# Performance work log

Measured on AMD Instinct MI355X. Metric: run time of the kernel, lower is better.

The kernel has to match this reference:

```python
import jax, jax.numpy as jnp
import numpy as np

VOCAB, DIM, B, S = 32000, 1024, 64, 512

def setup_inputs() -> dict:
    key = jax.random.key(0)
    ks = jax.random.split(key, 16)
    std = 1.0 / np.sqrt(DIM)
    return {
        "x": jax.random.randint(ks[0], (B,), 0, VOCAB),
        "h": jax.random.normal(ks[1], (B, DIM), jnp.float32),
        "c": jax.random.normal(ks[2], (B, DIM), jnp.float32),
        "enc_y": jax.random.normal(ks[3], (B, S, DIM), jnp.float32),
        "F_emb": jax.random.normal(ks[4], (VOCAB, DIM), jnp.float32),
        "W1_w": jax.random.uniform(ks[5], (DIM, DIM), jnp.float32, -std, std),
        "W1_b": jnp.zeros((DIM,), jnp.float32),
        "W2_w": jax.random.uniform(ks[6], (DIM, DIM), jnp.float32, -std, std),
        "W2_b": jnp.zeros((DIM,), jnp.float32),
        "V_w": jax.random.uniform(ks[7], (1, DIM), jnp.float32, -std, std),
        "V_b": jnp.zeros((1,), jnp.float32),
        "W_ih": jax.random.uniform(ks[8], (4 * DIM, DIM), jnp.float32, -std, std),
        "W_hh": jax.random.uniform(ks[9], (4 * DIM, DIM), jnp.float32, -std, std),
        "b_ih": jax.random.uniform(ks[10], (4 * DIM,), jnp.float32, -std, std),
        "b_hh": jax.random.uniform(ks[11], (4 * DIM,), jnp.float32, -std, std),
        "fc_w": jax.random.uniform(ks[12], (VOCAB, DIM), jnp.float32, -std, std),
        "fc_b": jnp.zeros((VOCAB,), jnp.float32),
    }

def reference(x, h, c, enc_y, F_emb, W1_w, W1_b, W2_w, W2_b, V_w, V_b,
              W_ih, W_hh, b_ih, b_hh, fc_w, fc_b):
    # Bahdanau additive attention (weights returned; context is dead code for layer=1)
    i_s = jnp.einsum('bsd,ed->bse', enc_y, W1_w) + W1_b          # [B,S,D]
    j_s = (h @ W2_w.T + W2_b)[:, None, :]                        # [B,1,D]
    score = jnp.tanh(i_s + j_s)                                  # [B,S,D]
    att = jax.nn.softmax(score @ V_w.T + V_b, axis=1)            # [B,S,1]
    # embedding lookup for the step token
    emb = F_emb[x]                                               # [B,D]
    # single-step LSTM (pytorch gate order: i, f, g, o)
    gates = emb @ W_ih.T + b_ih + h @ W_hh.T + b_hh              # [B,4D]
    ig, fg, gg, og = jnp.split(gates, 4, axis=-1)
    c_new = jax.nn.sigmoid(fg) * c + jax.nn.sigmoid(ig) * jnp.tanh(gg)
    h_new = jax.nn.sigmoid(og) * jnp.tanh(c_new)
    out = h_new + emb                                            # residual skip
    logits = out @ fc_w.T + fc_b                                 # [B,VOCAB]
    return logits, h_new, c_new, att
```

## Files before the change

### kernel.cpp

```cpp
#include <hip/hip_runtime.h>

#define DEV __device__ __forceinline__

typedef __bf16 bf16_t;
typedef bf16_t bf16x8 __attribute__((ext_vector_type(8)));
typedef float f32x4 __attribute__((ext_vector_type(4)));

static constexpr int VOCAB = 32000, DIM = 1024, BATCH = 64, SEQ = 512;
static constexpr int M_SC = BATCH * SEQ;

DEV unsigned short f2bf(float f) {
  unsigned u = __builtin_bit_cast(unsigned, f);
  u += 0x7FFFu + ((u >> 16) & 1u);
  return (unsigned short)(u >> 16);
}

DEV float sigmf(float x) {
  x = fminf(fmaxf(x, -30.f), 30.f);
  return 1.0f / (1.0f + __expf(-x));
}

DEV float tanh_fast(float x) {
  x = fminf(fmaxf(x, -20.f), 20.f);
  float e = __expf(2.0f * x);
  return (e - 1.0f) / (e + 1.0f);
}

DEV void gload_lds16(const void* g, void* l) {
  __builtin_amdgcn_global_load_lds(
      (__attribute__((address_space(1))) void*)(g),
      (__attribute__((address_space(3))) void*)(l), 16, 0, 0);
}

__global__ void __launch_bounds__(256) k_prep(const float* __restrict__ enc,
                                              const float* __restrict__ w1,
                                              unsigned short* __restrict__ enc_b,
                                              unsigned short* __restrict__ w1_b,
                                              float* __restrict__ att_l,
                                              const int* __restrict__ x,
                                              const float* __restrict__ Femb,
                                              const float* __restrict__ h,
                                              float* __restrict__ emb_f,
                                              unsigned short* __restrict__ eh_b,
                                              unsigned short* __restrict__ h_b) {
  if (blockIdx.x >= 1984) {
    int b = blockIdx.x - 1984;
    int tok = x[b];
    for (int d = threadIdx.x; d < DIM; d += 256) {
      float e = Femb[(size_t)tok * DIM + d];
      float hv = h[b * DIM + d];
      emb_f[b * DIM + d] = e;
      unsigned short eb = f2bf(e), hb = f2bf(hv);
      eh_b[b * 2 * DIM + d] = eb;
      eh_b[b * 2 * DIM + DIM + d] = hb;
      h_b[b * DIM + d] = hb;
    }
  }
  int gid = blockIdx.x * 256 + threadIdx.x;
  if (gid < M_SC) att_l[gid] = 0.f;
  const int ENC4 = (M_SC * DIM) / 4;
  const int TOT4 = ENC4 + (DIM * DIM) / 4;
  int stride = gridDim.x * 256;
  for (int i = gid; i < TOT4; i += stride) {
    float4 v;
    unsigned short* dst;
    if (i < ENC4) {
      v = ((const float4*)enc)[i];
      dst = enc_b + (size_t)i * 4;
    } else {
      v = ((const float4*)w1)[i - ENC4];
      dst = w1_b + (size_t)(i - ENC4) * 4;
    }
    ushort4 o;
    o.x = f2bf(v.x); o.y = f2bf(v.y); o.z = f2bf(v.z); o.w = f2bf(v.w);
    *(ushort4*)dst = o;
  }
}

__global__ void __launch_bounds__(256) k_skinny(
    const unsigned short* __restrict__ A1p, int lda1,
    const float* __restrict__ B1a, const float* __restrict__ B1b, int ksplit1,
    const float* __restrict__ bias1, float* __restrict__ C1, int N1, int K1,
    int nb1,
    const unsigned short* __restrict__ A2p, int lda2,
    const float* __restrict__ B2a, const float* __restrict__ B2b, int ksplit2,
    const float* __restrict__ bias2, float* __restrict__ C2, int N2, int K2) {
  __shared__ unsigned short As[2][64 * 128];
  __shared__ unsigned short Bs[2][16 * 128];
  int t = threadIdx.x;
  int l = t & 63, w = t >> 6;

  const unsigned short* A;
  const float *B1, *B2, *bias;
  float* C;
  int lda, ksplit, N, K, n0;
  if ((int)blockIdx.x < nb1) {
    A = A1p; lda = lda1; B1 = B1a; B2 = B1b; ksplit = ksplit1;
    bias = bias1; C = C1; N = N1; K = K1; n0 = blockIdx.x * 16;
  } else {
    A = A2p; lda = lda2; B1 = B2a; B2 = B2b; ksplit = ksplit2;
    bias = bias2; C = C2; N = N2; K = K2; n0 = (blockIdx.x - nb1) * 16;
  }

  f32x4 acc = {};
  int rx = (l & 7) << 3;

  float4 vB[2];

  auto loadB = [&](int k0) {
    const float* Bsrc;
    int kk;
    if (k0 < ksplit) { Bsrc = B1; kk = k0; } else { Bsrc = B2; kk = k0 - ksplit; }
#pragma unroll
    for (int i = 0; i < 2; ++i) {
      int lin = i * 256 + t;
      int row = lin >> 5, c4 = (lin & 31) * 4;
      vB[i] = *(const float4*)(Bsrc + (size_t)(n0 + row) * 1024 + kk + c4);
    }
  };
  auto writeB = [&](int bufi) {
#pragma unroll
    for (int i = 0; i < 2; ++i) {
      int lin = i * 256 + t;
      int row = lin >> 5, c4 = (lin & 31) * 4;
      ushort4 o;
      o.x = f2bf(vB[i].x); o.y = f2bf(vB[i].y); o.z = f2bf(vB[i].z); o.w = f2bf(vB[i].w);
      *(ushort4*)&Bs[bufi][row * 128 + (c4 ^ ((row & 7) << 3))] = o;
    }
  };
  auto stageA = [&](int k0, int bufi) {
#pragma unroll
    for (int i = 0; i < 4; ++i) {
      int sbase = i * 256 + w * 64;
      int s = sbase + l;
      int row = s >> 4;
      int scol = ((s & 15) ^ (row & 7)) * 8;
      gload_lds16(A + (size_t)row * lda + k0 + scol, &As[bufi][sbase * 8]);
    }
  };
  auto compute = [&](int bufi) {
#pragma unroll
    for (int kf = 0; kf < 4; ++kf) {
      int ko = kf * 32 + 8 * (l >> 4);
      int ar = w * 16 + (l & 15);
      bf16x8 af = *(const bf16x8*)&As[bufi][ar * 128 + (ko ^ rx)];
      bf16x8 bf = *(const bf16x8*)&Bs[bufi][(l & 15) * 128 + (ko ^ rx)];
      acc = __builtin_amdgcn_mfma_f32_16x16x32_bf16(af, bf, acc, 0, 0, 0);
    }
  };

  loadB(0);
  stageA(0, 0);
  writeB(0);
  asm volatile("s_waitcnt lgkmcnt(0)" ::: "memory");

  int nk = K / 128;
  int cur = 0;
  for (int kt = 0; kt < nk - 1; ++kt) {
    loadB((kt + 1) * 128);
    stageA((kt + 1) * 128, cur ^ 1);
    asm volatile("s_waitcnt vmcnt(6)\n\ts_barrier" ::: "memory");
    compute(cur);
    writeB(cur ^ 1);
    asm volatile("s_waitcnt lgkmcnt(0)\n\ts_barrier" ::: "memory");
    cur ^= 1;
  }
  asm volatile("s_waitcnt vmcnt(0)\n\ts_barrier" ::: "memory");
  compute(cur);

  int cn = n0 + (l & 15);
  float bv = bias ? bias[cn] : 0.f;
#pragma unroll
  for (int r = 0; r < 4; ++r) {
    int m = w * 16 + (l >> 4) * 4 + r;
    C[(size_t)m * N + cn] = acc[r] + bv;
  }
}

__global__ void __launch_bounds__(256) k_skinny32(
    const unsigned short* __restrict__ A,
    const float* __restrict__ B, const float* __restrict__ bias,
    float* __restrict__ C, int N, int K) {
  __shared__ unsigned short As[2][64 * 128];
  __shared__ unsigned short Bs[2][32 * 128];
  int t = threadIdx.x;
  int l = t & 63, w = t >> 6;
  int n0 = blockIdx.x * 32;
  f32x4 acc0 = {}, acc1 = {};
  int rx = (l & 7) << 3;

  float4 vB[4];

  auto loadB = [&](int k0) {
#pragma unroll
    for (int i = 0; i < 4; ++i) {
      int lin = i * 256 + t;
      int row = lin >> 5, c4 = (lin & 31) * 4;
      vB[i] = *(const float4*)(B + (size_t)(n0 + row) * 1024 + k0 + c4);
    }
  };
  auto writeB = [&](int bufi) {
#pragma unroll
    for (int i = 0; i < 4; ++i) {
      int lin = i * 256 + t;
      int row = lin >> 5, c4 = (lin & 31) * 4;
      ushort4 o;
      o.x = f2bf(vB[i].x); o.y = f2bf(vB[i].y); o.z = f2bf(vB[i].z); o.w = f2bf(vB[i].w);
      *(ushort4*)&Bs[bufi][row * 128 + (c4 ^ ((row & 7) << 3))] = o;
    }
  };
  auto stageA = [&](int k0, int bufi) {
#pragma unroll
    for (int i = 0; i < 4; ++i) {
      int sbase = i * 256 + w * 64;
      int s = sbase + l;
      int row = s >> 4;
      int scol = ((s & 15) ^ (row & 7)) * 8;
      gload_lds16(A + (size_t)row * DIM + k0 + scol, &As[bufi][sbase * 8]);
    }
  };
  auto compute = [&](int bufi) {
#pragma unroll
    for (int kf = 0; kf < 4; ++kf) {
      int ko = kf * 32 + 8 * (l >> 4);
      int ar = w * 16 + (l & 15);
      bf16x8 af = *(const bf16x8*)&As[bufi][ar * 128 + (ko ^ rx)];
      bf16x8 b0 = *(const bf16x8*)&Bs[bufi][(l & 15) * 128 + (ko ^ rx)];
      bf16x8 b1 = *(const bf16x8*)&Bs[bufi][((l & 15) + 16) * 128 + (ko ^ rx)];
      acc0 = __builtin_amdgcn_mfma_f32_16x16x32_bf16(af, b0, acc0, 0, 0, 0);
      acc1 = __builtin_amdgcn_mfma_f32_16x16x32_bf16(af, b1, acc1, 0, 0, 0);
    }
  };

  loadB(0);
  stageA(0, 0);
  writeB(0);
  asm volatile("s_waitcnt lgkmcnt(0)" ::: "memory");

  int nk = K / 128;
  int cur = 0;
  for (int kt = 0; kt < nk - 1; ++kt) {
    loadB((kt + 1) * 128);
    stageA((kt + 1) * 128, cur ^ 1);
    asm volatile("s_waitcnt vmcnt(8)\n\ts_barrier" ::: "memory");
    compute(cur);
    writeB(cur ^ 1);
    asm volatile("s_waitcnt lgkmcnt(0)\n\ts_barrier" ::: "memory");
    cur ^= 1;
  }
  asm volatile("s_waitcnt vmcnt(0)\n\ts_barrier" ::: "memory");
  compute(cur);

  int cn = n0 + (l & 15);
  float bv0 = bias ? bias[cn] : 0.f;
  float bv1 = bias ? bias[cn + 16] : 0.f;
#pragma unroll
  for (int r = 0; r < 4; ++r) {
    int m = w * 16 + (l >> 4) * 4 + r;
    C[(size_t)m * N + cn] = acc0[r] + bv0;
    C[(size_t)m * N + cn + 16] = acc1[r] + bv1;
  }
}

#define READ_A(MH)                                                              \
  do {                                                                          \
    _Pragma("unroll") for (int mf = 0; mf < 4; ++mf)                            \
    _Pragma("unroll") for (int kk = 0; kk < 2; ++kk) {                          \
      int row_ = wm * 128 + (MH) * 64 + mf * 16 + lm;                           \
      fa[mf][kk] = *(const bf16x8*)&As[ct][row_ * 64 + ((kk * 32 + 8 * lq) ^ rx)]; \
    }                                                                           \
  } while (0)
#define READ_B(NH)                                                              \
  do {                                                                          \
    _Pragma("unroll") for (int nf = 0; nf < 2; ++nf)                            \
    _Pragma("unroll") for (int kk = 0; kk < 2; ++kk) {                          \
      int row_ = wn * 64 + (NH) * 32 + nf * 16 + lm;                            \
      fb[NH][nf][kk] = *(const bf16x8*)&Bs[ct][row_ * 64 + ((kk * 32 + 8 * lq) ^ rx)]; \
    }                                                                           \
  } while (0)
#define MFMA_Q(MH, NH)                                                          \
  do {                                                                          \
    __builtin_amdgcn_s_setprio(1);                                              \
    _Pragma("unroll") for (int mf = 0; mf < 4; ++mf)                            \
    _Pragma("unroll") for (int nf = 0; nf < 2; ++nf)                            \
    _Pragma("unroll") for (int kk = 0; kk < 2; ++kk)                            \
        acc[(MH) * 4 + mf][(NH) * 2 + nf] = __builtin_amdgcn_mfma_f32_16x16x32_bf16( \
            fa[mf][kk], fb[NH][nf][kk], acc[(MH) * 4 + mf][(NH) * 2 + nf], 0, 0, 0); \
    __builtin_amdgcn_s_setprio(0);                                              \
  } while (0)

__global__ void __launch_bounds__(512, 2) k_score(
    const unsigned short* __restrict__ encb, const unsigned short* __restrict__ w1mat,
    const float* __restrict__ js, const float* __restrict__ w1bias,
    const float* __restrict__ vw, float* __restrict__ att_l) {
  __shared__ unsigned short As[2][256 * 64];
  __shared__ unsigned short Bs[2][256 * 64];
  int tid = threadIdx.x;
  int lane = tid & 63, wid = tid >> 6;
  int wm = wid >> 2, wn = wid & 3;
  int lm = lane & 15, lq = lane >> 4;
  int rx = (lane & 7) << 3;

  int wg = blockIdx.x;
  int swz = (wg & 7) * 64 + (wg >> 3);
  int m0 = (swz >> 2) * 256;
  int n0 = (swz & 3) * 256;

  const unsigned short* pa = encb + (size_t)m0 * DIM;
  const unsigned short* pb = w1mat + (size_t)n0 * DIM;

  f32x4 acc[8][4] = {};
  bf16x8 fa[4][2];
  bf16x8 fb[2][2][2];

  auto stageA = [&](int kt, int h, int bufi) {
#pragma unroll
    for (int i = 0; i < 2; ++i) {
      int rowbase = i * 128 + h * 64 + wid * 8;
      int row = rowbase + (lane >> 3);
      int scol = ((lane & 7) ^ (row & 7)) * 8;
      gload_lds16(pa + (size_t)row * DIM + kt * 64 + scol, &As[bufi][rowbase * 64]);
    }
  };
  auto stageB = [&](int kt, int h, int bufi) {
#pragma unroll
    for (int i = 0; i < 2; ++i) {
      int j0 = i * 64 + wid * 8;
      int rowbase = (j0 >> 5) * 64 + h * 32 + (j0 & 31);
      int row = rowbase + (lane >> 3);
      int scol = ((lane & 7) ^ (row & 7)) * 8;
      gload_lds16(pb + (size_t)row * DIM + kt * 64 + scol, &Bs[bufi][rowbase * 64]);
    }
  };

  stageA(0, 0, 0);
  stageB(0, 0, 0);
  stageB(0, 1, 0);
  stageA(0, 1, 0);
  asm volatile("s_waitcnt vmcnt(4)\n\ts_barrier" ::: "memory");

  for (int t = 0; t < 15; ++t) {
    const int ct = t & 1;
    READ_A(0); READ_B(0);
    stageA(t + 1, 0, ct ^ 1);
    asm volatile("s_waitcnt vmcnt(4)\n\ts_barrier" ::: "memory");
    MFMA_Q(0, 0);
    asm volatile("s_barrier" ::: "memory");
    READ_B(1);
    stageB(t + 1, 0, ct ^ 1);
    asm volatile("s_waitcnt vmcnt(4)\n\ts_barrier" ::: "memory");
    MFMA_Q(0, 1);
    asm volatile("s_barrier" ::: "memory");
    READ_A(1);
    stageB(t + 1, 1, ct ^ 1);
    asm volatile("s_barrier" ::: "memory");
    MFMA_Q(1, 1);
    asm volatile("s_barrier" ::: "memory");
    stageA(t + 1, 1, ct ^ 1);
    asm volatile("s_waitcnt vmcnt(4)\n\ts_barrier" ::: "memory");
    MFMA_Q(1, 0);
    asm volatile("s_barrier" ::: "memory");
  }
  {
    const int ct = 1;
    READ_A(0); READ_B(0);
    asm volatile("s_waitcnt vmcnt(2)\n\ts_barrier" ::: "memory");
    MFMA_Q(0, 0);
    asm volatile("s_barrier" ::: "memory");
    READ_B(1);
    asm volatile("s_waitcnt vmcnt(0)\n\ts_barrier" ::: "memory");
    MFMA_Q(0, 1);
    asm volatile("s_barrier" ::: "memory");
    READ_A(1);
    MFMA_Q(1, 1);
    MFMA_Q(1, 0);
  }

  int b = m0 >> 9;
  const float* jrow = js + b * DIM;
  float jvv[4], vvv[4];
#pragma unroll
  for (int nj = 0; nj < 4; ++nj) {
    int e = n0 + wn * 64 + nj * 16 + lm;
    jvv[nj] = jrow[e] + w1bias[e];
    vvv[nj] = vw[e];
  }
#pragma unroll
  for (int mi = 0; mi < 8; ++mi) {
    float psum[4] = {0.f, 0.f, 0.f, 0.f};
#pragma unroll
    for (int nj = 0; nj < 4; ++nj)
#pragma unroll
      for (int r = 0; r < 4; ++r)
        psum[r] += tanh_fast(acc[mi][nj][r] + jvv[nj]) * vvv[nj];
#pragma unroll
    for (int r = 0; r < 4; ++r) {
      float s = psum[r];
      s += __shfl_xor(s, 1);
      s += __shfl_xor(s, 2);
      s += __shfl_xor(s, 4);
      s += __shfl_xor(s, 8);
      if (lm == 0)
        atomicAdd(&att_l[m0 + wm * 128 + mi * 16 + lq * 4 + r], s);
    }
  }
}
#undef READ_A
#undef READ_B
#undef MFMA_Q

__global__ void __launch_bounds__(256) k_lstm(
    const float* __restrict__ gates, const float* __restrict__ bih,
    const float* __restrict__ bhh, const float* __restrict__ c,
    const float* __restrict__ emb_f, float* __restrict__ out_h,
    float* __restrict__ out_c, unsigned short* __restrict__ out_b,
    const float* __restrict__ att_l, float* __restrict__ att) {
  if (blockIdx.x >= 256) {
    __shared__ float red[8];
    int b = blockIdx.x - 256;
    int t = threadIdx.x;
    float v0 = att_l[b * SEQ + t];
    float v1 = att_l[b * SEQ + t + 256];
    float m = fmaxf(v0, v1);
#pragma unroll
    for (int o = 32; o; o >>= 1) m = fmaxf(m, __shfl_xor(m, o));
    if ((t & 63) == 0) red[t >> 6] = m;
    __syncthreads();
    m = fmaxf(fmaxf(red[0], red[1]), fmaxf(red[2], red[3]));
    float e0 = __expf(v0 - m), e1 = __expf(v1 - m);
    float s = e0 + e1;
#pragma unroll
    for (int o = 32; o; o >>= 1) s += __shfl_xor(s, o);
    __syncthreads();
    if ((t & 63) == 0) red[4 + (t >> 6)] = s;
    __syncthreads();
    s = red[4] + red[5] + red[6] + red[7];
    att[b * SEQ + t] = e0 / s;
    att[b * SEQ + t + 256] = e1 / s;
    return;
  }
  int t = blockIdx.x * 256 + threadIdx.x;
  int b = t >> 10, d = t & 1023;
  const float* g = gates + b * 4 * DIM;
  float ig = g[d] + bih[d] + bhh[d];
  float fg = g[DIM + d] + bih[DIM + d] + bhh[DIM + d];
  float gg = g[2 * DIM + d] + bih[2 * DIM + d] + bhh[2 * DIM + d];
  float og = g[3 * DIM + d] + bih[3 * DIM + d] + bhh[3 * DIM + d];
  float cn = sigmf(fg) * c[t] + sigmf(ig) * tanh_fast(gg);
  float hn = sigmf(og) * tanh_fast(cn);
  out_h[t] = hn;
  out_c[t] = cn;
  out_b[t] = f2bf(hn + emb_f[t]);
}

extern "C" void kernel_launch(void* const* d_in, const int* in_sizes, int n_in,
                              void* d_out, int out_size, void* d_ws, size_t ws_size,
                              hipStream_t stream) {
  const int* x = (const int*)d_in[0];
  const float* h = (const float*)d_in[1];
  const float* c = (const float*)d_in[2];
  const float* enc = (const float*)d_in[3];
  const float* Femb = (const float*)d_in[4];
  const float* W1w = (const float*)d_in[5];
  const float* W1b = (const float*)d_in[6];
  const float* W2w = (const float*)d_in[7];
  const float* W2b = (const float*)d_in[8];
  const float* Vw = (const float*)d_in[9];
  const float* Wih = (const float*)d_in[11];
  const float* Whh = (const float*)d_in[12];
  const float* bih = (const float*)d_in[13];
  const float* bhh = (const float*)d_in[14];
  const float* fcw = (const float*)d_in[15];
  const float* fcb = (const float*)d_in[16];

  float* out_logits = (float*)d_out;
  float* out_h = out_logits + (size_t)BATCH * VOCAB;
  float* out_c = out_h + BATCH * DIM;
  float* out_att = out_c + BATCH * DIM;

  char* p = (char*)d_ws;
  unsigned short* enc_b = (unsigned short*)p; p += (size_t)M_SC * DIM * 2;
  unsigned short* w1_b = (unsigned short*)p;  p += (size_t)DIM * DIM * 2;
  float* att_l = (float*)p;                   p += (size_t)M_SC * 4;
  float* js = (float*)p;                      p += (size_t)BATCH * DIM * 4;
  float* emb_f = (float*)p;                   p += (size_t)BATCH * DIM * 4;
  unsigned short* eh_b = (unsigned short*)p;  p += (size_t)BATCH * 2 * DIM * 2;
  unsigned short* h_b = (unsigned short*)p;   p += (size_t)BATCH * DIM * 2;
  float* gates = (float*)p;                   p += (size_t)BATCH * 4 * DIM * 4;
  unsigned short* out_b = (unsigned short*)p; p += (size_t)BATCH * DIM * 2;

  hipLaunchKernelGGL(k_prep, dim3(2048), dim3(256), 0, stream, enc, W1w, enc_b, w1_b,
                     att_l, x, Femb, h, emb_f, eh_b, h_b);
  hipLaunchKernelGGL(k_skinny, dim3(256 + 64), dim3(256), 0, stream,
                     eh_b, 2 * DIM, Wih, Whh, DIM, (const float*)nullptr,
                     gates, 4 * DIM, 2 * DIM,
                     256,
                     h_b, DIM, W2w, W2w, DIM, W2b, js, DIM, DIM);
  hipLaunchKernelGGL(k_score, dim3(512), dim3(512), 0, stream,
                     enc_b, w1_b, js, W1b, Vw, att_l);
  hipLaunchKernelGGL(k_lstm, dim3(320), dim3(256), 0, stream,
                     gates, bih, bhh, c, emb_f, out_h, out_c, out_b, att_l, out_att);
  hipLaunchKernelGGL(k_skinny32, dim3(VOCAB / 32), dim3(256), 0, stream,
                     out_b, fcw, fcb, out_logits, VOCAB, DIM);
}
```

Baseline: 169.4 us.

## Process two M tiles per workgroup in k_score with continuous K-pipeline

```diff
diff --git a/kernel.cpp b/kernel.cpp
--- a/kernel.cpp
+++ b/kernel.cpp
@@ -302,24 +302,25 @@
   int rx = (lane & 7) << 3;
 
   int wg = blockIdx.x;
-  int swz = (wg & 7) * 64 + (wg >> 3);
+  int swz = (wg & 7) * 32 + (wg >> 3);
   int m0 = (swz >> 2) * 256;
   int n0 = (swz & 3) * 256;
 
   const unsigned short* pa = encb + (size_t)m0 * DIM;
+  const unsigned short* pa2 = encb + (size_t)(m0 + 16384) * DIM;
   const unsigned short* pb = w1mat + (size_t)n0 * DIM;
 
   f32x4 acc[8][4] = {};
   bf16x8 fa[4][2];
   bf16x8 fb[2][2][2];
 
-  auto stageA = [&](int kt, int h, int bufi) {
+  auto stageA = [&](const unsigned short* pax, int kt, int h, int bufi) {
 #pragma unroll
     for (int i = 0; i < 2; ++i) {
       int rowbase = i * 128 + h * 64 + wid * 8;
       int row = rowbase + (lane >> 3);
       int scol = ((lane & 7) ^ (row & 7)) * 8;
-      gload_lds16(pa + (size_t)row * DIM + kt * 64 + scol, &As[bufi][rowbase * 64]);
+      gload_lds16(pax + (size_t)row * DIM + kt * 64 + scol, &As[bufi][rowbase * 64]);
     }
   };
   auto stageB = [&](int kt, int h, int bufi) {
@@ -332,34 +333,74 @@
       gload_lds16(pb + (size_t)row * DIM + kt * 64 + scol, &Bs[bufi][rowbase * 64]);
     }
   };
-
-  stageA(0, 0, 0);
+  auto epilogue = [&](int m0p) {
+    int b = m0p >> 9;
+    const float* jrow = js + b * DIM;
+    float jvv[4], vvv[4];
+#pragma unroll
+    for (int nj = 0; nj < 4; ++nj) {
+      int e = n0 + wn * 64 + nj * 16 + lm;
+      jvv[nj] = jrow[e] + w1bias[e];
+      vvv[nj] = vw[e];
+    }
+#pragma unroll
+    for (int mi = 0; mi < 8; ++mi) {
+      float psum[4] = {0.f, 0.f, 0.f, 0.f};
+#pragma unroll
+      for (int nj = 0; nj < 4; ++nj)
+#pragma unroll
+        for (int r = 0; r < 4; ++r)
+          psum[r] += tanh_fast(acc[mi][nj][r] + jvv[nj]) * vvv[nj];
+#pragma unroll
+      for (int r = 0; r < 4; ++r) {
+        float s = psum[r];
+        s += __shfl_xor(s, 1);
+        s += __shfl_xor(s, 2);
+        s += __shfl_xor(s, 4);
+        s += __shfl_xor(s, 8);
+        if (lm == 0)
+          atomicAdd(&att_l[m0p + wm * 128 + mi * 16 + lq * 4 + r], s);
+      }
+    }
+  };
+
+  stageA(pa, 0, 0, 0);
   stageB(0, 0, 0);
   stageB(0, 1, 0);
-  stageA(0, 1, 0);
+  stageA(pa, 0, 1, 0);
   asm volatile("s_waitcnt vmcnt(4)\n\ts_barrier" ::: "memory");
 
-  for (int t = 0; t < 15; ++t) {
+  for (int t = 0; t < 31; ++t) {
     const int ct = t & 1;
+    const int nkt = (t + 1) & 15;
+    const unsigned short* pax = (t + 1 < 16) ? pa : pa2;
     READ_A(0); READ_B(0);
-    stageA(t + 1, 0, ct ^ 1);
+    stageA(pax, nkt, 0, ct ^ 1);
     asm volatile("s_waitcnt vmcnt(4)\n\ts_barrier" ::: "memory");
     MFMA_Q(0, 0);
     asm volatile("s_barrier" ::: "memory");
     READ_B(1);
-    stageB(t + 1, 0, ct ^ 1);
+    stageB(nkt, 0, ct ^ 1);
     asm volatile("s_waitcnt vmcnt(4)\n\ts_barrier" ::: "memory");
     MFMA_Q(0, 1);
     asm volatile("s_barrier" ::: "memory");
     READ_A(1);
-    stageB(t + 1, 1, ct ^ 1);
+    stageB(nkt, 1, ct ^ 1);
     asm volatile("s_barrier" ::: "memory");
     MFMA_Q(1, 1);
     asm volatile("s_barrier" ::: "memory");
-    stageA(t + 1, 1, ct ^ 1);
+    stageA(pax, nkt, 1, ct ^ 1);
     asm volatile("s_waitcnt vmcnt(4)\n\ts_barrier" ::: "memory");
     MFMA_Q(1, 0);
     asm volatile("s_barrier" ::: "memory");
+    if (t == 15) {
+      epilogue(m0);
+#pragma unroll
+      for (int i = 0; i < 8; ++i)
+#pragma unroll
+        for (int j = 0; j < 4; ++j)
+          acc[i][j] = f32x4{0.f, 0.f, 0.f, 0.f};
+    }
   }
   {
     const int ct = 1;
@@ -375,35 +416,7 @@
     MFMA_Q(1, 1);
     MFMA_Q(1, 0);
   }
-
-  int b = m0 >> 9;
-  const float* jrow = js + b * DIM;
-  float jvv[4], vvv[4];
-#pragma unroll
-  for (int nj = 0; nj < 4; ++nj) {
-    int e = n0 + wn * 64 + nj * 16 + lm;
-    jvv[nj] = jrow[e] + w1bias[e];
-    vvv[nj] = vw[e];
-  }
-#pragma unroll
-  for (int mi = 0; mi < 8; ++mi) {
-    float psum[4] = {0.f, 0.f, 0.f, 0.f};
-#pragma unroll
-    for (int nj = 0; nj < 4; ++nj)
-#pragma unroll
-      for (int r = 0; r < 4; ++r)
-        psum[r] += tanh_fast(acc[mi][nj][r] + jvv[nj]) * vvv[nj];
-#pragma unroll
-    for (int r = 0; r < 4; ++r) {
-      float s = psum[r];
-      s += __shfl_xor(s, 1);
-      s += __shfl_xor(s, 2);
-      s += __shfl_xor(s, 4);
-      s += __shfl_xor(s, 8);
-      if (lm == 0)
-        atomicAdd(&att_l[m0 + wm * 128 + mi * 16 + lq * 4 + r], s);
-    }
-  }
+  epilogue(m0 + 16384);
 }
 #undef READ_A
 #undef READ_B
@@ -496,7 +509,7 @@
                      gates, 4 * DIM, 2 * DIM,
                      256,
                      h_b, DIM, W2w, W2w, DIM, W2b, js, DIM, DIM);
-  hipLaunchKernelGGL(k_score, dim3(512), dim3(512), 0, stream,
+  hipLaunchKernelGGL(k_score, dim3(256), dim3(512), 0, stream,
                      enc_b, w1_b, js, W1b, Vw, att_l);
   hipLaunchKernelGGL(k_lstm, dim3(320), dim3(256), 0, stream,
                      gates, bih, bhh, c, emb_f, out_h, out_c, out_b, att_l, out_att);
```

Result: slower. 183.8 us (+8.5%).
